# Optimization experiments

Hardware: AMD Instinct MI355X
Metric: run time of the kernel (lower is better)

Reference implementation:

```python
import jax, jax.numpy as jnp
import numpy as np

N_FEATURES = 256
SEQ_LEN = 128
N_HIDDEN = 30
N_LAYERS = 2
BATCH = 1024


def _lstm_layer(x, w_ih, w_hh, b_ih, b_hh):
    # x: [B, T, I]; w_ih: [4H, I]; w_hh: [4H, H]; biases: [4H]
    # PyTorch gate order: i, f, g, o
    B = x.shape[0]
    H = w_hh.shape[1]
    # precompute input contribution for all timesteps: [B, T, 4H]
    xg = jnp.einsum('bti,gi->btg', x, w_ih) + (b_ih + b_hh)
    xg = jnp.swapaxes(xg, 0, 1)  # [T, B, 4H]

    def step(carry, xg_t):
        h, c = carry
        gates = xg_t + h @ w_hh.T  # [B, 4H]
        i, f, g, o = jnp.split(gates, 4, axis=-1)
        i = jax.nn.sigmoid(i)
        f = jax.nn.sigmoid(f)
        g = jnp.tanh(g)
        o = jax.nn.sigmoid(o)
        c = f * c + i * g
        h = o * jnp.tanh(c)
        return (h, c), h

    h0 = jnp.zeros((B, H), dtype=x.dtype)
    c0 = jnp.zeros((B, H), dtype=x.dtype)
    _, hs = jax.lax.scan(step, (h0, c0), xg)
    return jnp.swapaxes(hs, 0, 1)  # [B, T, H]


def setup_inputs() -> dict:
    key = jax.random.key(0)
    ks = jax.random.split(key, 12)
    s_in = 1.0 / np.sqrt(N_HIDDEN)
    G = 4 * N_HIDDEN
    inp = {
        'x': jax.random.normal(ks[0], (BATCH, SEQ_LEN, N_FEATURES), dtype=jnp.float32),
        'w_ih0': jax.random.uniform(ks[1], (G, N_FEATURES), jnp.float32, -s_in, s_in),
        'w_hh0': jax.random.uniform(ks[2], (G, N_HIDDEN), jnp.float32, -s_in, s_in),
        'b_ih0': jax.random.uniform(ks[3], (G,), jnp.float32, -s_in, s_in),
        'b_hh0': jax.random.uniform(ks[4], (G,), jnp.float32, -s_in, s_in),
        'w_ih1': jax.random.uniform(ks[5], (G, N_HIDDEN), jnp.float32, -s_in, s_in),
        'w_hh1': jax.random.uniform(ks[6], (G, N_HIDDEN), jnp.float32, -s_in, s_in),
        'b_ih1': jax.random.uniform(ks[7], (G,), jnp.float32, -s_in, s_in),
        'b_hh1': jax.random.uniform(ks[8], (G,), jnp.float32, -s_in, s_in),
        'w_lin': jax.random.uniform(ks[9], (1, N_HIDDEN * SEQ_LEN), jnp.float32, -s_in, s_in),
        'b_lin': jax.random.uniform(ks[10], (1,), jnp.float32, -s_in, s_in),
    }
    return inp


def reference(x, w_ih0, w_hh0, b_ih0, b_hh0, w_ih1, w_hh1, b_ih1, b_hh1, w_lin, b_lin):
    h1 = _lstm_layer(x, w_ih0, w_hh0, b_ih0, b_hh0)   # [B, T, H]
    h2 = _lstm_layer(h1, w_ih1, w_hh1, b_ih1, b_hh1)  # [B, T, H]
    flat = h2.reshape(h2.shape[0], -1)                 # [B, T*H]
    return flat @ w_lin.T + b_lin                      # [B, 1]
```

## Files before the change

kernel.cpp:

```cpp
#include <hip/hip_runtime.h>

#define T_SEQ 128
#define NF 256
#define NH 30
#define NG 120
#define NBATCH 1024
#define M_ROWS (NBATCH * T_SEQ)

#define BIAS_OFF 0
#define BHI_OFF  1024
#define BLO_OFF  (BHI_OFF + 65536)
#define XG_OFF_B (BLO_OFF + 65536)

typedef __attribute__((ext_vector_type(8))) short short8;
typedef __attribute__((ext_vector_type(4))) float float4v;

__device__ __forceinline__ short bf16_of(float f) {
  union { float f; unsigned u; } v; v.f = f;
  unsigned r = v.u + 0x7fffu + ((v.u >> 16) & 1u);
  return (short)(r >> 16);
}
__device__ __forceinline__ float f_of_bf16(short s) {
  union { unsigned u; float f; } v; v.u = ((unsigned)(unsigned short)s) << 16;
  return v.f;
}

__device__ __forceinline__ float rl(float v, int j) {
  return __int_as_float(__builtin_amdgcn_readlane(__float_as_int(v), j));
}
__device__ __forceinline__ float fast_rcp(float x) { return __builtin_amdgcn_rcpf(x); }
__device__ __forceinline__ float act_mix(float x, float kIn, float kOut, float cOut) {
  float e = __expf(-kIn * x);
  float r = fast_rcp(1.0f + e);
  return fmaf(kOut, r, cOut);
}
__device__ __forceinline__ float tanh_fast(float x) {
  float e = __expf(-2.0f * x);
  float r = fast_rcp(1.0f + e);
  return fmaf(2.0f, r, -1.0f);
}

__global__ void prep_kernel(const float* __restrict__ w_ih0,
                            const float* __restrict__ b_ih0,
                            const float* __restrict__ b_hh0,
                            unsigned char* __restrict__ ws) {
  int gid = blockIdx.x * 256 + threadIdx.x;
  float* bias = (float*)(ws + BIAS_OFF);
  if (gid < 128) bias[gid] = (gid < NG) ? (b_ih0[gid] + b_hh0[gid]) : 0.0f;

  int lane = gid & 63;
  int ts = gid >> 6;
  int t = ts >> 3, s = ts & 7;
  int n = s * 16 + (lane & 15);
  int k0 = t * 32 + (lane >> 4) * 8;

  short8 hi, lo;
#pragma unroll
  for (int j = 0; j < 8; ++j) {
    float v = (n < NG) ? w_ih0[n * NF + k0 + j] : 0.0f;
    short h = bf16_of(v);
    hi[j] = h;
    lo[j] = bf16_of(v - f_of_bf16(h));
  }
  *(short8*)(ws + BHI_OFF + (size_t)gid * 16) = hi;
  *(short8*)(ws + BLO_OFF + (size_t)gid * 16) = lo;
}

__global__ __launch_bounds__(256, 3) void gemm_xg(const float* __restrict__ x,
                                                  const unsigned char* __restrict__ ws,
                                                  float* __restrict__ xg) {
  __shared__ short lds_B[2][8 * 2 * 64 * 8];
  const int tid = threadIdx.x;
  const int lane = tid & 63;
  const int wave = tid >> 6;
  const int r15 = lane & 15;
  const int quad = lane >> 4;
  const int rowbase = blockIdx.x * 128 + wave * 32;

  const short* __restrict__ Bhi = (const short*)(ws + BHI_OFF);
  const short* __restrict__ Blo = (const short*)(ws + BLO_OFF);
  const float* __restrict__ bias = (const float*)(ws + BIAS_OFF);

  float4v acc[2][8];
#pragma unroll
  for (int s = 0; s < 8; ++s) {
    float b = bias[s * 16 + r15];
    float4v bv = {b, b, b, b};
    acc[0][s] = bv;
    acc[1][s] = bv;
  }

  const float* xptr[2];
  xptr[0] = x + (size_t)(rowbase + r15) * NF + quad * 8;
  xptr[1] = x + (size_t)(rowbase + 16 + r15) * NF + quad * 8;

#pragma unroll
  for (int i = 0; i < 2; ++i) {
    int s = wave * 2 + i;
    const short* ghi = Bhi + ((size_t)(0 * 8 + s) * 64 + lane) * 8;
    const short* glo = Blo + ((size_t)(0 * 8 + s) * 64 + lane) * 8;
    short* lhi = &lds_B[0][(s * 2 + 0) * 64 * 8];
    short* llo = &lds_B[0][(s * 2 + 1) * 64 * 8];
    __builtin_amdgcn_global_load_lds((const __attribute__((address_space(1))) void*)ghi,
                                     (__attribute__((address_space(3))) void*)lhi, 16, 0, 0);
    __builtin_amdgcn_global_load_lds((const __attribute__((address_space(1))) void*)glo,
                                     (__attribute__((address_space(3))) void*)llo, 16, 0, 0);
  }

  short8 ahi[2], alo[2];
#pragma unroll
  for (int g = 0; g < 2; ++g) {
    float4 p0 = *(const float4*)(xptr[g] + 0);
    float4 p1 = *(const float4*)(xptr[g] + 4);
    float f[8] = {p0.x, p0.y, p0.z, p0.w, p1.x, p1.y, p1.z, p1.w};
#pragma unroll
    for (int j = 0; j < 8; ++j) {
      short h = bf16_of(f[j]);
      ahi[g][j] = h;
      alo[g][j] = bf16_of(f[j] - f_of_bf16(h));
    }
  }
  __syncthreads();

  for (int t = 0; t < 8; ++t) {
    const int buf = t & 1;
    float4 anx[2][2];
    if (t < 7) {
#pragma unroll
      for (int i = 0; i < 2; ++i) {
        int s = wave * 2 + i;
        const short* ghi = Bhi + ((size_t)((t + 1) * 8 + s) * 64 + lane) * 8;
        const short* glo = Blo + ((size_t)((t + 1) * 8 + s) * 64 + lane) * 8;
        short* lhi = &lds_B[buf ^ 1][(s * 2 + 0) * 64 * 8];
        short* llo = &lds_B[buf ^ 1][(s * 2 + 1) * 64 * 8];
        __builtin_amdgcn_global_load_lds((const __attribute__((address_space(1))) void*)ghi,
                                         (__attribute__((address_space(3))) void*)lhi, 16, 0, 0);
        __builtin_amdgcn_global_load_lds((const __attribute__((address_space(1))) void*)glo,
                                         (__attribute__((address_space(3))) void*)llo, 16, 0, 0);
      }
#pragma unroll
      for (int g = 0; g < 2; ++g) {
        anx[g][0] = *(const float4*)(xptr[g] + (t + 1) * 32);
        anx[g][1] = *(const float4*)(xptr[g] + (t + 1) * 32 + 4);
      }
    }

#pragma unroll
    for (int s = 0; s < 8; ++s) {
      const short8 bh = *(const short8*)&lds_B[buf][((s * 2 + 0) * 64 + lane) * 8];
      const short8 bl = *(const short8*)&lds_B[buf][((s * 2 + 1) * 64 + lane) * 8];
#pragma unroll
      for (int g = 0; g < 2; ++g) {
        acc[g][s] = __builtin_amdgcn_mfma_f32_16x16x32_bf16(ahi[g], bh, acc[g][s], 0, 0, 0);
        acc[g][s] = __builtin_amdgcn_mfma_f32_16x16x32_bf16(ahi[g], bl, acc[g][s], 0, 0, 0);
        acc[g][s] = __builtin_amdgcn_mfma_f32_16x16x32_bf16(alo[g], bh, acc[g][s], 0, 0, 0);
      }
    }

    if (t < 7) {
#pragma unroll
      for (int g = 0; g < 2; ++g) {
        float f[8] = {anx[g][0].x, anx[g][0].y, anx[g][0].z, anx[g][0].w,
                      anx[g][1].x, anx[g][1].y, anx[g][1].z, anx[g][1].w};
#pragma unroll
        for (int j = 0; j < 8; ++j) {
          short h = bf16_of(f[j]);
          ahi[g][j] = h;
          alo[g][j] = bf16_of(f[j] - f_of_bf16(h));
        }
      }
    }
    __syncthreads();
  }

#pragma unroll
  for (int g = 0; g < 2; ++g) {
    const int row0 = rowbase + g * 16 + quad * 4;
#pragma unroll
    for (int s = 0; s < 8; ++s) {
      const int col = s * 16 + r15;
      if (col < NG) {
#pragma unroll
        for (int i = 0; i < 4; ++i) {
          xg[(size_t)(row0 + i) * NG + col] = acc[g][s][i];
        }
      }
    }
  }
}

__global__ __launch_bounds__(64) void lstm_fused(const float* __restrict__ xg,
                                                 const float* __restrict__ w_hh0,
                                                 const float* __restrict__ w_ih1,
                                                 const float* __restrict__ w_hh1,
                                                 const float* __restrict__ b_ih1,
                                                 const float* __restrict__ b_hh1,
                                                 const float* __restrict__ w_lin,
                                                 const float* __restrict__ b_lin,
                                                 float* __restrict__ out) {
  const int b = blockIdx.x;
  const int lane = threadIdx.x;
  const bool hiHalf = lane >= 32;
  const int l = hiHalf ? (lane - 32) : lane;
  const int lc = (l < NH) ? l : (NH - 1);
  const int gA = hiHalf ? (60 + lc) : lc;
  const int gB = gA + NH;

  const float kInA = hiHalf ? 2.0f : 1.0f;
  const float kOutA = hiHalf ? 2.0f : 1.0f;
  const float cOutA = hiHalf ? -1.0f : 0.0f;

  float wA0[NH], wB0[NH], vA1[NH], vB1[NH], uA1[NH], uB1[NH];
#pragma unroll
  for (int j = 0; j < NH; ++j) {
    wA0[j] = w_hh0[gA * NH + j];
    wB0[j] = w_hh0[gB * NH + j];
    vA1[j] = w_ih1[gA * NH + j];
    vB1[j] = w_ih1[gB * NH + j];
    uA1[j] = w_hh1[gA * NH + j];
    uB1[j] = w_hh1[gB * NH + j];
  }
  const float bA1 = b_ih1[gA] + b_hh1[gA];
  const float bB1 = b_ih1[gB] + b_hh1[gB];

  float h0 = 0.0f, c0 = 0.0f, h1 = 0.0f, c1 = 0.0f, acc = 0.0f;
  const float* __restrict__ xgb = xg + (size_t)b * T_SEQ * NG;

  float xa[4], xb[4], wlr[4];
#pragma unroll
  for (int p = 0; p < 3; ++p) {
    xa[p] = xgb[p * NG + gA];
    xb[p] = xgb[p * NG + gB];
    wlr[p] = w_lin[p * NH + lc];
  }

#pragma unroll 4
  for (int t = 0; t < T_SEQ; ++t) {
    const int cur = t & 3;
    const int nxt = (t + 3) & 3;
    const int tp = (t + 3 < T_SEQ) ? (t + 3) : (T_SEQ - 1);
    float pxa = xgb[tp * NG + gA];
    float pxb = xgb[tp * NG + gB];
    float pwl = w_lin[tp * NH + lc];

    float sA = xa[cur], sB = xb[cur], sA2 = 0.0f, sB2 = 0.0f;
#pragma unroll
    for (int j = 0; j < NH; j += 2) {
      float hj = rl(h0, j);
      float hj1 = rl(h0, j + 1);
      sA = fmaf(hj, wA0[j], sA);
      sB = fmaf(hj, wB0[j], sB);
      sA2 = fmaf(hj1, wA0[j + 1], sA2);
      sB2 = fmaf(hj1, wB0[j + 1], sB2);
    }
    sA += sA2;
    sB += sB2;
    float aA = act_mix(sA, kInA, kOutA, cOutA);
    float aB = act_mix(sB, 1.0f, 1.0f, 0.0f);
    float gg = __shfl_down(aA, 32);
    float oo = __shfl_down(aB, 32);
    c0 = fmaf(aB, c0, aA * gg);
    h0 = oo * tanh_fast(c0);

    float sv = bA1, sv2 = 0.0f, svB = bB1, svB2 = 0.0f;
    float su = 0.0f, su2 = 0.0f, suB = 0.0f, suB2 = 0.0f;
#pragma unroll
    for (int j = 0; j < NH; j += 2) {
      float xj = rl(h0, j);
      float xj1 = rl(h0, j + 1);
      float hj = rl(h1, j);
      float hj1 = rl(h1, j + 1);
      sv = fmaf(xj, vA1[j], sv);
      svB = fmaf(xj, vB1[j], svB);
      sv2 = fmaf(xj1, vA1[j + 1], sv2);
      svB2 = fmaf(xj1, vB1[j + 1], svB2);
      su = fmaf(hj, uA1[j], su);
      suB = fmaf(hj, uB1[j], suB);
      su2 = fmaf(hj1, uA1[j + 1], su2);
      suB2 = fmaf(hj1, uB1[j + 1], suB2);
    }
    float s1A = (sv + sv2) + (su + su2);
    float s1B = (svB + svB2) + (suB + suB2);
    float a1A = act_mix(s1A, kInA, kOutA, cOutA);
    float a1B = act_mix(s1B, 1.0f, 1.0f, 0.0f);
    float gg1 = __shfl_down(a1A, 32);
    float oo1 = __shfl_down(a1B, 32);
    c1 = fmaf(a1B, c1, a1A * gg1);
    h1 = oo1 * tanh_fast(c1);

    acc = fmaf(h1, wlr[cur], acc);

    xa[nxt] = pxa;
    xb[nxt] = pxb;
    wlr[nxt] = pwl;
  }

  if (lane >= NH) acc = 0.0f;
#pragma unroll
  for (int off = 32; off > 0; off >>= 1) acc += __shfl_xor(acc, off);
  if (lane == 0) out[b] = acc + b_lin[0];
}

extern "C" void kernel_launch(void* const* d_in, const int* in_sizes, int n_in,
                              void* d_out, int out_size, void* d_ws, size_t ws_size,
                              hipStream_t stream) {
  (void)in_sizes; (void)n_in; (void)out_size; (void)ws_size;
  const float* x     = (const float*)d_in[0];
  const float* w_ih0 = (const float*)d_in[1];
  const float* w_hh0 = (const float*)d_in[2];
  const float* b_ih0 = (const float*)d_in[3];
  const float* b_hh0 = (const float*)d_in[4];
  const float* w_ih1 = (const float*)d_in[5];
  const float* w_hh1 = (const float*)d_in[6];
  const float* b_ih1 = (const float*)d_in[7];
  const float* b_hh1 = (const float*)d_in[8];
  const float* w_lin = (const float*)d_in[9];
  const float* b_lin = (const float*)d_in[10];
  unsigned char* ws = (unsigned char*)d_ws;
  float* out = (float*)d_out;
  float* xg = (float*)(ws + XG_OFF_B);

  prep_kernel<<<16, 256, 0, stream>>>(w_ih0, b_ih0, b_hh0, ws);
  gemm_xg<<<M_ROWS / 128, 256, 0, stream>>>(x, ws, xg);
  lstm_fused<<<NBATCH, 64, 0, stream>>>(xg, w_hh0, w_ih1, w_hh1,
                                        b_ih1, b_hh1, w_lin, b_lin, out);
}
```

Measured before the change: 291.5 us.

## Skew layer-0 recurrence one step ahead to share broadcasts with layer 1

Layer 0's step t+1 is now computed in the same loop iteration as layer 1's step t. Both consume h0(t), so the lane broadcasts of h0 are issued once and reused by both matvecs, and the two dependency chains become independent and can interleave. This shortens the serial critical path per timestep and removes duplicate readlane work. The cost is more live accumulators and registers, the prefetch distance shrinks from three steps to one, and the launch bounds now request a minimum of one block.

```diff
diff --git a/kernel.cpp b/kernel.cpp
--- a/kernel.cpp
+++ b/kernel.cpp
@@ -189,15 +189,15 @@
   }
 }
 
-__global__ __launch_bounds__(64) void lstm_fused(const float* __restrict__ xg,
-                                                 const float* __restrict__ w_hh0,
-                                                 const float* __restrict__ w_ih1,
-                                                 const float* __restrict__ w_hh1,
-                                                 const float* __restrict__ b_ih1,
-                                                 const float* __restrict__ b_hh1,
-                                                 const float* __restrict__ w_lin,
-                                                 const float* __restrict__ b_lin,
-                                                 float* __restrict__ out) {
+__global__ __launch_bounds__(64, 1) void lstm_fused(const float* __restrict__ xg,
+                                                    const float* __restrict__ w_hh0,
+                                                    const float* __restrict__ w_ih1,
+                                                    const float* __restrict__ w_hh1,
+                                                    const float* __restrict__ b_ih1,
+                                                    const float* __restrict__ b_hh1,
+                                                    const float* __restrict__ w_lin,
+                                                    const float* __restrict__ b_lin,
+                                                    float* __restrict__ out) {
   const int b = blockIdx.x;
   const int lane = threadIdx.x;
   const bool hiHalf = lane >= 32;
@@ -223,63 +223,48 @@
   const float bA1 = b_ih1[gA] + b_hh1[gA];
   const float bB1 = b_ih1[gB] + b_hh1[gB];
 
-  float h0 = 0.0f, c0 = 0.0f, h1 = 0.0f, c1 = 0.0f, acc = 0.0f;
   const float* __restrict__ xgb = xg + (size_t)b * T_SEQ * NG;
 
-  float xa[4], xb[4], wlr[4];
-#pragma unroll
-  for (int p = 0; p < 3; ++p) {
-    xa[p] = xgb[p * NG + gA];
-    xb[p] = xgb[p * NG + gB];
-    wlr[p] = w_lin[p * NH + lc];
-  }
-
-#pragma unroll 4
+  float a0A = act_mix(xgb[gA], kInA, kOutA, cOutA);
+  float a0B = act_mix(xgb[gB], 1.0f, 1.0f, 0.0f);
+  float gg0 = __shfl_down(a0A, 32);
+  float oo0 = __shfl_down(a0B, 32);
+  float c0 = a0A * gg0;
+  float h0 = oo0 * tanh_fast(c0);
+  float h1 = 0.0f, c1 = 0.0f, acc = 0.0f;
+  float wl_cur = w_lin[lc];
+
+#pragma unroll 2
   for (int t = 0; t < T_SEQ; ++t) {
-    const int cur = t & 3;
-    const int nxt = (t + 3) & 3;
-    const int tp = (t + 3 < T_SEQ) ? (t + 3) : (T_SEQ - 1);
-    float pxa = xgb[tp * NG + gA];
-    float pxb = xgb[tp * NG + gB];
-    float pwl = w_lin[tp * NH + lc];
-
-    float sA = xa[cur], sB = xb[cur], sA2 = 0.0f, sB2 = 0.0f;
-#pragma unroll
-    for (int j = 0; j < NH; j += 2) {
-      float hj = rl(h0, j);
-      float hj1 = rl(h0, j + 1);
-      sA = fmaf(hj, wA0[j], sA);
-      sB = fmaf(hj, wB0[j], sB);
-      sA2 = fmaf(hj1, wA0[j + 1], sA2);
-      sB2 = fmaf(hj1, wB0[j + 1], sB2);
-    }
-    sA += sA2;
-    sB += sB2;
-    float aA = act_mix(sA, kInA, kOutA, cOutA);
-    float aB = act_mix(sB, 1.0f, 1.0f, 0.0f);
-    float gg = __shfl_down(aA, 32);
-    float oo = __shfl_down(aB, 32);
-    c0 = fmaf(aB, c0, aA * gg);
-    h0 = oo * tanh_fast(c0);
-
-    float sv = bA1, sv2 = 0.0f, svB = bB1, svB2 = 0.0f;
-    float su = 0.0f, su2 = 0.0f, suB = 0.0f, suB2 = 0.0f;
+    const int tn = (t + 1 < T_SEQ) ? (t + 1) : (T_SEQ - 1);
+    float xnA = xgb[tn * NG + gA];
+    float xnB = xgb[tn * NG + gB];
+    float wl_nxt = w_lin[tn * NH + lc];
+
+    float svA = bA1, svA2 = 0.0f, svB = bB1, svB2 = 0.0f;
+    float suA = 0.0f, suA2 = 0.0f, suB = 0.0f, suB2 = 0.0f;
+    float snA = 0.0f, snA2 = 0.0f, snB = 0.0f, snB2 = 0.0f;
 #pragma unroll
     for (int j = 0; j < NH; j += 2) {
       float xj = rl(h0, j);
       float xj1 = rl(h0, j + 1);
       float hj = rl(h1, j);
       float hj1 = rl(h1, j + 1);
-      sv = fmaf(xj, vA1[j], sv);
+      svA = fmaf(xj, vA1[j], svA);
       svB = fmaf(xj, vB1[j], svB);
-      sv2 = fmaf(xj1, vA1[j + 1], sv2);
+      suA = fmaf(hj, uA1[j], suA);
+      suB = fmaf(hj, uB1[j], suB);
+      snA = fmaf(xj, wA0[j], snA);
+      snB = fmaf(xj, wB0[j], snB);
+      svA2 = fmaf(xj1, vA1[j + 1], svA2);
       svB2 = fmaf(xj1, vB1[j + 1], svB2);
-      su = fmaf(hj, uA1[j], su);
-      suB = fmaf(hj, uB1[j], suB);
-      su2 = fmaf(hj1, uA1[j + 1], su2);
+      suA2 = fmaf(hj1, uA1[j + 1], suA2);
       suB2 = fmaf(hj1, uB1[j + 1], suB2);
-    }
-    float s1A = (sv + sv2) + (su + su2);
+      snA2 = fmaf(xj1, wA0[j + 1], snA2);
+      snB2 = fmaf(xj1, wB0[j + 1], snB2);
+    }
+
+    float s1A = (svA + svA2) + (suA + suA2);
     float s1B = (svB + svB2) + (suB + suB2);
     float a1A = act_mix(s1A, kInA, kOutA, cOutA);
     float a1B = act_mix(s1B, 1.0f, 1.0f, 0.0f);
@@ -287,12 +272,18 @@
     float oo1 = __shfl_down(a1B, 32);
     c1 = fmaf(a1B, c1, a1A * gg1);
     h1 = oo1 * tanh_fast(c1);
-
-    acc = fmaf(h1, wlr[cur], acc);
-
-    xa[nxt] = pxa;
-    xb[nxt] = pxb;
-    wlr[nxt] = pwl;
+    acc = fmaf(h1, wl_cur, acc);
+
+    float s0A = (snA + snA2) + xnA;
+    float s0B = (snB + snB2) + xnB;
+    a0A = act_mix(s0A, kInA, kOutA, cOutA);
+    a0B = act_mix(s0B, 1.0f, 1.0f, 0.0f);
+    gg0 = __shfl_down(a0A, 32);
+    oo0 = __shfl_down(a0B, 32);
+    c0 = fmaf(a0B, c0, a0A * gg0);
+    h0 = oo0 * tanh_fast(c0);
+
+    wl_cur = wl_nxt;
   }
 
   if (lane >= NH) acc = 0.0f;
```

Result: slower. 303.7 us (+4.2%).
